# Optimization experiments

Measured on AMD Instinct MI355X. Metric: run time of the kernel, lower is better.

Reference implementation:

```python
import jax, jax.numpy as jnp
import numpy as np

N_NODES = 100000
N_EDGES = 1000000
NUM_GRAPHS = 500
EPS = 1e-5


def gcn_conv(x, src, dst, W, b, n_nodes):
    # PyG GCNConv: h = x @ W, symmetric norm with self-loops, aggregate at dst, add bias
    h = x @ W
    deg = jnp.zeros((n_nodes,), h.dtype).at[dst].add(1.0) + 1.0  # in-degree + self-loop
    dis = jax.lax.rsqrt(deg)
    msg = h[src] * (dis[src] * dis[dst])[:, None]               # [E, F] gather
    agg = jnp.zeros_like(h).at[dst].add(msg)                    # scatter-add
    return agg + h * (dis * dis)[:, None] + b                   # self-loop term + bias


def bn_eval(x, g, be, m, v):
    return (x - m) * jax.lax.rsqrt(v + EPS) * g + be


def setup_inputs() -> dict:
    key = jax.random.key(0)
    ks = jax.random.split(key, 8)
    edge_index = jax.random.randint(ks[0], (2, N_EDGES), 0, N_NODES, dtype=jnp.int32)
    batch = jnp.sort(jax.random.randint(ks[1], (N_NODES,), 0, NUM_GRAPHS, dtype=jnp.int32))
    d_in, h1, h2, hc, nc = 64, 64, 32, 16, 2
    return {
        "x": jax.random.normal(ks[2], (N_NODES, d_in), jnp.float32),
        "edge_index": edge_index,
        "batch": batch,
        "W1": jax.random.normal(ks[3], (d_in, h1), jnp.float32) / np.sqrt(d_in),
        "b1": jnp.zeros((h1,), jnp.float32),
        "g1": jnp.ones((h1,), jnp.float32),
        "be1": jnp.zeros((h1,), jnp.float32),
        "m1": jnp.zeros((h1,), jnp.float32),
        "v1": jnp.ones((h1,), jnp.float32),
        "W2": jax.random.normal(ks[4], (h1, h2), jnp.float32) / np.sqrt(h1),
        "b2": jnp.zeros((h2,), jnp.float32),
        "g2": jnp.ones((h2,), jnp.float32),
        "be2": jnp.zeros((h2,), jnp.float32),
        "m2": jnp.zeros((h2,), jnp.float32),
        "v2": jnp.ones((h2,), jnp.float32),
        "Wc1": jax.random.normal(ks[5], (h2, hc), jnp.float32) / np.sqrt(h2),
        "bc1": jnp.zeros((hc,), jnp.float32),
        "Wc2": jax.random.normal(ks[6], (hc, nc), jnp.float32) / np.sqrt(hc),
        "bc2": jnp.zeros((nc,), jnp.float32),
    }


def reference(x, edge_index, batch, W1, b1, g1, be1, m1, v1,
              W2, b2, g2, be2, m2, v2, Wc1, bc1, Wc2, bc2):
    src, dst = edge_index[0], edge_index[1]
    n = x.shape[0]
    # encoder layer 1: GCNConv -> BN(eval) -> ReLU  (dropout off in eval)
    h = jax.nn.relu(bn_eval(gcn_conv(x, src, dst, W1, b1, n), g1, be1, m1, v1))
    # encoder layer 2
    h = jax.nn.relu(bn_eval(gcn_conv(h, src, dst, W2, b2, n), g2, be2, m2, v2))
    # global mean pool over graphs
    sums = jax.ops.segment_sum(h, batch, num_segments=NUM_GRAPHS)
    cnts = jax.ops.segment_sum(jnp.ones((n,), h.dtype), batch, num_segments=NUM_GRAPHS)
    z = sums / jnp.maximum(cnts, 1.0)[:, None]                  # [NUM_GRAPHS, h2]
    # classifier MLP
    return jax.nn.relu(z @ Wc1 + bc1) @ Wc2 + bc2               # [NUM_GRAPHS, num_classes]
```

## Files before the change

kernel.cpp:

```cpp
#include <hip/hip_runtime.h>
#include <hip/hip_bf16.h>


#define CHUNK 4096
#define CAP   4096

typedef float floatx2 __attribute__((ext_vector_type(2)));

__global__ void k_zero_misc(int* __restrict__ bucketCursor, float* __restrict__ sums,
                            int nSums) {
    int i = blockIdx.x * blockDim.x + threadIdx.x;
    if (i < 512) bucketCursor[i] = 0;
    int j = i - 512;
    if (j >= 0 && j < nSums) sums[j] = 0.f;
}

__global__ __launch_bounds__(256) void k_binpairs2(
    const int* __restrict__ src, const int* __restrict__ dst,
    int* __restrict__ bucketCursor, unsigned* __restrict__ pairs, int E) {
    __shared__ int lh[512];
    __shared__ int lbase[512];
    for (int i = threadIdx.x; i < 512; i += 256) lh[i] = 0;
    __syncthreads();
    int base = blockIdx.x * CHUNK;
    for (int i = threadIdx.x; i < CHUNK; i += 256) {
        int e = base + i;
        if (e < E) atomicAdd(&lh[dst[e] >> 8], 1);
    }
    __syncthreads();
    for (int i = threadIdx.x; i < 512; i += 256) {
        int c = lh[i];
        lbase[i] = c ? atomicAdd(&bucketCursor[i], c) : 0;
        lh[i] = 0;
    }
    __syncthreads();
    for (int i = threadIdx.x; i < CHUNK; i += 256) {
        int e = base + i;
        if (e < E) {
            int d = dst[e];
            int b = d >> 8;
            int r = atomicAdd(&lh[b], 1);
            pairs[(size_t)b * CAP + lbase[b] + r] =
                ((unsigned)src[e] << 8) | (unsigned)(d & 255);
        }
    }
}

__global__ __launch_bounds__(256) void k_csr2(
    const unsigned* __restrict__ pairs, const int* __restrict__ bucketCursor,
    int* __restrict__ rowStart, int* __restrict__ rowEnd,
    float* __restrict__ dis, int* __restrict__ perm, int n) {
    __shared__ int cnt[256];
    __shared__ int s[256];
    __shared__ int cur[256];
    int b = blockIdx.x, tid = threadIdx.x;
    int total = bucketCursor[b];
    size_t base = (size_t)b * CAP;
    cnt[tid] = 0;
    __syncthreads();
    for (int i = tid; i < total; i += 256) atomicAdd(&cnt[pairs[base + i] & 255], 1);
    __syncthreads();
    int v = cnt[tid];
    s[tid] = v;
    __syncthreads();
    for (int off = 1; off < 256; off <<= 1) {
        int t = (tid >= off) ? s[tid - off] : 0;
        __syncthreads();
        s[tid] += t;
        __syncthreads();
    }
    int excl = s[tid] - v;
    int node = b * 256 + tid;
    if (node < n) {
        rowStart[node] = (int)base + excl;
        rowEnd[node]   = (int)base + excl + v;
        dis[node] = rsqrtf((float)v + 1.0f);
    }
    cur[tid] = excl;
    __syncthreads();
    for (int i = tid; i < total; i += 256) {
        unsigned pr = pairs[base + i];
        int lo = pr & 255;
        int slot = atomicAdd(&cur[lo], 1);
        perm[base + slot] = (int)(pr >> 8);
    }
}

__global__ __launch_bounds__(256) void k_gemm64(
    const float* __restrict__ x, const float* __restrict__ W,
    const float* __restrict__ dis, unsigned char* __restrict__ hs8, int n) {
    __shared__ float Ws[64 * 64];
    __shared__ float xs[128][65];
    const int tid = threadIdx.x;
    for (int i = tid * 4; i < 4096; i += 1024)
        *(float4*)&Ws[i] = *(const float4*)&W[i];
    const int base = blockIdx.x * 128;
    for (int i = tid; i < 2048; i += 256) {
        int r = i >> 4;
        int k = (i & 15) * 4;
        int row = base + r;
        float4 xv = (row < n) ? *(const float4*)&x[(size_t)row * 64 + k]
                              : make_float4(0.f, 0.f, 0.f, 0.f);
        xs[r][k] = xv.x; xs[r][k + 1] = xv.y; xs[r][k + 2] = xv.z; xs[r][k + 3] = xv.w;
    }
    __syncthreads();
    const int cg = tid & 7;
    const int rg = tid >> 3;
    float acc[4][8] = {};
#pragma unroll 4
    for (int k = 0; k < 64; ++k) {
        float w8[8];
        *(float4*)&w8[0] = *(const float4*)&Ws[k * 64 + cg * 8];
        *(float4*)&w8[4] = *(const float4*)&Ws[k * 64 + cg * 8 + 4];
        float x4[4];
#pragma unroll
        for (int rr = 0; rr < 4; ++rr) x4[rr] = xs[rg * 4 + rr][k];
#pragma unroll
        for (int rr = 0; rr < 4; ++rr)
#pragma unroll
            for (int cc = 0; cc < 8; ++cc)
                acc[rr][cc] = fmaf(x4[rr], w8[cc], acc[rr][cc]);
    }
#pragma unroll
    for (int rr = 0; rr < 4; ++rr) {
        int row = base + rg * 4 + rr;
        if (row >= n) break;
        float d = dis[row];
        int q0 = __builtin_amdgcn_cvt_pk_fp8_f32(acc[rr][0] * d, acc[rr][1] * d, 0, false);
        q0 = __builtin_amdgcn_cvt_pk_fp8_f32(acc[rr][2] * d, acc[rr][3] * d, q0, true);
        int q1 = __builtin_amdgcn_cvt_pk_fp8_f32(acc[rr][4] * d, acc[rr][5] * d, 0, false);
        q1 = __builtin_amdgcn_cvt_pk_fp8_f32(acc[rr][6] * d, acc[rr][7] * d, q1, true);
        uint2 q = {(unsigned)q0, (unsigned)q1};
        *(uint2*)&hs8[(size_t)row * 64 + cg * 8] = q;
    }
}

__device__ __forceinline__ void unpack8(uint2 u, float* a) {
    floatx2 p0 = __builtin_amdgcn_cvt_pk_f32_fp8(u.x, false);
    floatx2 p1 = __builtin_amdgcn_cvt_pk_f32_fp8(u.x, true);
    floatx2 p2 = __builtin_amdgcn_cvt_pk_f32_fp8(u.y, false);
    floatx2 p3 = __builtin_amdgcn_cvt_pk_f32_fp8(u.y, true);
    a[0] = p0[0]; a[1] = p0[1]; a[2] = p1[0]; a[3] = p1[1];
    a[4] = p2[0]; a[5] = p2[1]; a[6] = p3[0]; a[7] = p3[1];
}

__global__ __launch_bounds__(256) void k_g64f8_gemm32(
    const unsigned char* __restrict__ hs8, const int* __restrict__ rowStart,
    const int* __restrict__ rowEnd, const int* __restrict__ perm,
    const float* __restrict__ dis,
    const float* __restrict__ b, const float* __restrict__ g,
    const float* __restrict__ be, const float* __restrict__ m,
    const float* __restrict__ v, const float* __restrict__ W2,
    unsigned char* __restrict__ hs2f8, int n) {
    __shared__ float W2s[64 * 32];
    __shared__ float actS[32][68];
    for (int i = threadIdx.x * 4; i < 2048; i += 1024)
        *(float4*)&W2s[i] = *(const float4*)&W2[i];
    __syncthreads();

    const uint2* hsu = (const uint2*)hs8;
    int c = threadIdx.x & 7;
    int ln = threadIdx.x >> 3;
    int node = (blockIdx.x * 256 + threadIdx.x) >> 3;
    if (node >= n) return;
    int r0 = rowStart[node], r1 = rowEnd[node];
    float d = dis[node];
    float a[8];
    unpack8(hsu[(size_t)node * 8 + c], a);
    int e = r0;
    for (; e + 7 < r1; e += 8) {
        int s0 = perm[e],     s1 = perm[e + 1], s2 = perm[e + 2], s3 = perm[e + 3];
        int s4 = perm[e + 4], s5 = perm[e + 5], s6 = perm[e + 6], s7 = perm[e + 7];
        uint2 u0 = hsu[(size_t)s0 * 8 + c];
        uint2 u1 = hsu[(size_t)s1 * 8 + c];
        uint2 u2 = hsu[(size_t)s2 * 8 + c];
        uint2 u3 = hsu[(size_t)s3 * 8 + c];
        uint2 u4 = hsu[(size_t)s4 * 8 + c];
        uint2 u5 = hsu[(size_t)s5 * 8 + c];
        uint2 u6 = hsu[(size_t)s6 * 8 + c];
        uint2 u7 = hsu[(size_t)s7 * 8 + c];
        float t[8];
#pragma unroll
        for (int j = 0; j < 8; ++j) {
            uint2 u = j == 0 ? u0 : j == 1 ? u1 : j == 2 ? u2 : j == 3 ? u3
                    : j == 4 ? u4 : j == 5 ? u5 : j == 6 ? u6 : u7;
            unpack8(u, t);
#pragma unroll
            for (int q = 0; q < 8; ++q) a[q] += t[q];
        }
    }
    for (; e < r1; ++e) {
        float t[8];
        unpack8(hsu[(size_t)perm[e] * 8 + c], t);
#pragma unroll
        for (int q = 0; q < 8; ++q) a[q] += t[q];
    }
    int f = 8 * c;
    float y[8];
#pragma unroll
    for (int h = 0; h < 2; ++h) {
        float4 gv = *(const float4*)&g[f + 4 * h];
        float4 vv = *(const float4*)&v[f + 4 * h];
        float4 bv = *(const float4*)&b[f + 4 * h];
        float4 mv = *(const float4*)&m[f + 4 * h];
        float4 bev = *(const float4*)&be[f + 4 * h];
        float sc0 = gv.x * rsqrtf(vv.x + 1e-5f), sc1 = gv.y * rsqrtf(vv.y + 1e-5f);
        float sc2 = gv.z * rsqrtf(vv.z + 1e-5f), sc3 = gv.w * rsqrtf(vv.w + 1e-5f);
        float y0 = fmaf(a[4 * h + 0] * d, sc0, (bv.x - mv.x) * sc0 + bev.x);
        float y1 = fmaf(a[4 * h + 1] * d, sc1, (bv.y - mv.y) * sc1 + bev.y);
        float y2 = fmaf(a[4 * h + 2] * d, sc2, (bv.z - mv.z) * sc2 + bev.z);
        float y3 = fmaf(a[4 * h + 3] * d, sc3, (bv.w - mv.w) * sc3 + bev.w);
        y[4 * h + 0] = y0 > 0.f ? y0 : 0.f;
        y[4 * h + 1] = y1 > 0.f ? y1 : 0.f;
        y[4 * h + 2] = y2 > 0.f ? y2 : 0.f;
        y[4 * h + 3] = y3 > 0.f ? y3 : 0.f;
    }
    *(float4*)&actS[ln][f]     = *(float4*)&y[0];
    *(float4*)&actS[ln][f + 4] = *(float4*)&y[4];

    float o0 = 0.f, o1 = 0.f, o2 = 0.f, o3 = 0.f;
#pragma unroll
    for (int k = 0; k < 64; ++k) {
        float av = actS[ln][k];
        float4 w = *(const float4*)&W2s[k * 32 + 4 * c];
        o0 = fmaf(av, w.x, o0);
        o1 = fmaf(av, w.y, o1);
        o2 = fmaf(av, w.z, o2);
        o3 = fmaf(av, w.w, o3);
    }
    int q = __builtin_amdgcn_cvt_pk_fp8_f32(o0 * d, o1 * d, 0, false);
    q = __builtin_amdgcn_cvt_pk_fp8_f32(o2 * d, o3 * d, q, true);
    *(unsigned*)&hs2f8[(size_t)node * 32 + 4 * c] = (unsigned)q;
}

__global__ __launch_bounds__(256) void k_g32f8_pool(
    const unsigned char* __restrict__ hs8, const int* __restrict__ rowStart,
    const int* __restrict__ rowEnd, const int* __restrict__ perm,
    const float* __restrict__ dis,
    const float* __restrict__ b, const float* __restrict__ g,
    const float* __restrict__ be, const float* __restrict__ m,
    const float* __restrict__ v, const int* __restrict__ batch,
    float* __restrict__ sums, float* __restrict__ cntG, int n) {
    __shared__ float lsum[64][32];
    __shared__ float lcnt[64];
    const uint2* hsu = (const uint2*)hs8;
    int tid = threadIdx.x;
    int c = tid & 3;
    int node = (blockIdx.x * 256 + tid) >> 2;
    int base = blockIdx.x * 64;
    bool valid = node < n;

    int lastNode = min(base + 63, n - 1);
    int g0 = batch[base < n ? base : n - 1];
    int span = batch[lastNode] - g0 + 1;
    bool ldsPath = span <= 64;

    if (ldsPath) {
        for (int i = tid; i < span * 32; i += 256) lsum[i >> 5][i & 31] = 0.f;
        for (int i = tid; i < span; i += 256) lcnt[i] = 0.f;
    }
    __syncthreads();

    float y[8];
    int f = 8 * c;
    int bg = 0;
    if (valid) {
        int r0 = rowStart[node], r1 = rowEnd[node];
        float d = dis[node];
        float a[8];
        unpack8(hsu[(size_t)node * 4 + c], a);
        int e = r0;
        for (; e + 7 < r1; e += 8) {
            int s0 = perm[e],     s1 = perm[e + 1], s2 = perm[e + 2], s3 = perm[e + 3];
            int s4 = perm[e + 4], s5 = perm[e + 5], s6 = perm[e + 6], s7 = perm[e + 7];
            uint2 u0 = hsu[(size_t)s0 * 4 + c];
            uint2 u1 = hsu[(size_t)s1 * 4 + c];
            uint2 u2 = hsu[(size_t)s2 * 4 + c];
            uint2 u3 = hsu[(size_t)s3 * 4 + c];
            uint2 u4 = hsu[(size_t)s4 * 4 + c];
            uint2 u5 = hsu[(size_t)s5 * 4 + c];
            uint2 u6 = hsu[(size_t)s6 * 4 + c];
            uint2 u7 = hsu[(size_t)s7 * 4 + c];
            float t[8];
#pragma unroll
            for (int j = 0; j < 8; ++j) {
                uint2 u = j == 0 ? u0 : j == 1 ? u1 : j == 2 ? u2 : j == 3 ? u3
                        : j == 4 ? u4 : j == 5 ? u5 : j == 6 ? u6 : u7;
                unpack8(u, t);
#pragma unroll
                for (int q = 0; q < 8; ++q) a[q] += t[q];
            }
        }
        for (; e < r1; ++e) {
            float t[8];
            unpack8(hsu[(size_t)perm[e] * 4 + c], t);
#pragma unroll
            for (int q = 0; q < 8; ++q) a[q] += t[q];
        }
#pragma unroll
        for (int h = 0; h < 2; ++h) {
            float4 gv = *(const float4*)&g[f + 4 * h];
            float4 vv = *(const float4*)&v[f + 4 * h];
            float4 bv = *(const float4*)&b[f + 4 * h];
            float4 mv = *(const float4*)&m[f + 4 * h];
            float4 bev = *(const float4*)&be[f + 4 * h];
            float sc0 = gv.x * rsqrtf(vv.x + 1e-5f), sc1 = gv.y * rsqrtf(vv.y + 1e-5f);
            float sc2 = gv.z * rsqrtf(vv.z + 1e-5f), sc3 = gv.w * rsqrtf(vv.w + 1e-5f);
            float y0 = fmaf(a[4 * h + 0] * d, sc0, (bv.x - mv.x) * sc0 + bev.x);
            float y1 = fmaf(a[4 * h + 1] * d, sc1, (bv.y - mv.y) * sc1 + bev.y);
            float y2 = fmaf(a[4 * h + 2] * d, sc2, (bv.z - mv.z) * sc2 + bev.z);
            float y3 = fmaf(a[4 * h + 3] * d, sc3, (bv.w - mv.w) * sc3 + bev.w);
            y[4 * h + 0] = y0 > 0.f ? y0 : 0.f;
            y[4 * h + 1] = y1 > 0.f ? y1 : 0.f;
            y[4 * h + 2] = y2 > 0.f ? y2 : 0.f;
            y[4 * h + 3] = y3 > 0.f ? y3 : 0.f;
        }
        bg = batch[node];
        if (ldsPath) {
            int gl = bg - g0;
#pragma unroll
            for (int j = 0; j < 8; ++j) atomicAdd(&lsum[gl][f + j], y[j]);
            if (c == 0) atomicAdd(&lcnt[gl], 1.f);
        } else {
#pragma unroll
            for (int j = 0; j < 8; ++j) atomicAdd(&sums[(size_t)bg * 32 + f + j], y[j]);
            if (c == 0) atomicAdd(&cntG[bg], 1.f);
        }
    }
    __syncthreads();
    if (ldsPath) {
        for (int i = tid; i < span * 32; i += 256) {
            int gs = i >> 5, ff = i & 31;
            float vl = lsum[gs][ff];
            if (vl != 0.f) atomicAdd(&sums[(size_t)(g0 + gs) * 32 + ff], vl);
        }
        for (int i = tid; i < span; i += 256) {
            float vl = lcnt[i];
            if (vl != 0.f) atomicAdd(&cntG[g0 + i], vl);
        }
    }
}

__global__ void k_mlp(const float* __restrict__ sums, const float* __restrict__ cnt,
                      const float* __restrict__ Wc1, const float* __restrict__ bc1,
                      const float* __restrict__ Wc2, const float* __restrict__ bc2,
                      float* __restrict__ out, int G) {
    int g = blockIdx.x * blockDim.x + threadIdx.x;
    if (g >= G) return;
    float c = cnt[g];
    c = c < 1.f ? 1.f : c;
    float inv = 1.f / c;
    float z[32];
#pragma unroll
    for (int j = 0; j < 32; ++j) z[j] = sums[(size_t)g * 32 + j] * inv;
    float o0 = bc2[0], o1 = bc2[1];
#pragma unroll
    for (int k = 0; k < 16; ++k) {
        float t = bc1[k];
#pragma unroll
        for (int j = 0; j < 32; ++j) t = fmaf(z[j], Wc1[j * 16 + k], t);
        t = t > 0.f ? t : 0.f;
        o0 = fmaf(t, Wc2[k * 2 + 0], o0);
        o1 = fmaf(t, Wc2[k * 2 + 1], o1);
    }
    out[g * 2 + 0] = o0;
    out[g * 2 + 1] = o1;
}

extern "C" void kernel_launch(void* const* d_in, const int* in_sizes, int n_in,
                              void* d_out, int out_size, void* d_ws, size_t ws_size,
                              hipStream_t stream) {
    const float* x   = (const float*)d_in[0];
    const int* ei    = (const int*)d_in[1];
    const int* batch = (const int*)d_in[2];
    const float* W1  = (const float*)d_in[3];
    const float* b1  = (const float*)d_in[4];
    const float* g1  = (const float*)d_in[5];
    const float* be1 = (const float*)d_in[6];
    const float* m1  = (const float*)d_in[7];
    const float* v1  = (const float*)d_in[8];
    const float* W2  = (const float*)d_in[9];
    const float* b2  = (const float*)d_in[10];
    const float* g2  = (const float*)d_in[11];
    const float* be2 = (const float*)d_in[12];
    const float* m2  = (const float*)d_in[13];
    const float* v2  = (const float*)d_in[14];
    const float* Wc1 = (const float*)d_in[15];
    const float* bc1 = (const float*)d_in[16];
    const float* Wc2 = (const float*)d_in[17];
    const float* bc2 = (const float*)d_in[18];

    const int n = in_sizes[2];
    const int E = in_sizes[1] / 2;
    const int G = out_size / 2;
    const int* srcI = ei;
    const int* dstI = ei + E;
    const int NB = (n + 255) >> 8;

    char* pw = (char*)d_ws;
    auto alloc = [&](size_t bytes) {
        char* r = pw;
        pw += (bytes + 255) & ~(size_t)255;
        return r;
    };
    float*    dis          = (float*)alloc((size_t)n * 4);
    int*      bucketCursor = (int*)alloc(512 * 4);
    unsigned* pairs        = (unsigned*)alloc((size_t)NB * CAP * 4);
    int*      perm         = (int*)alloc((size_t)NB * CAP * 4);
    int*      rowStart     = (int*)alloc((size_t)n * 4);
    int*      rowEnd       = (int*)alloc((size_t)n * 4);
    unsigned char* hs1f8   = (unsigned char*)alloc((size_t)64 * n);
    unsigned char* hs2f8   = (unsigned char*)alloc((size_t)32 * n);
    float*    sums         = (float*)alloc((size_t)32 * G * 4 + (size_t)G * 4);
    float*    cntG         = sums + (size_t)32 * G;

    const int NT = 256;
    const int nbE = (E + CHUNK - 1) / CHUNK;
    const int nSums = G * 33;

    k_zero_misc<<<(512 + nSums + NT - 1) / NT, NT, 0, stream>>>(bucketCursor, sums, nSums);
    k_binpairs2<<<nbE, NT, 0, stream>>>(srcI, dstI, bucketCursor, pairs, E);
    k_csr2<<<NB, NT, 0, stream>>>(pairs, bucketCursor, rowStart, rowEnd, dis, perm, n);

    k_gemm64<<<(n + 127) / 128, NT, 0, stream>>>(x, W1, dis, hs1f8, n);
    k_g64f8_gemm32<<<(n * 8 + NT - 1) / NT, NT, 0, stream>>>(
        hs1f8, rowStart, rowEnd, perm, dis, b1, g1, be1, m1, v1, W2, hs2f8, n);

    k_g32f8_pool<<<(n * 4 + NT - 1) / NT, NT, 0, stream>>>(
        hs2f8, rowStart, rowEnd, perm, dis, b2, g2, be2, m2, v2, batch,
        sums, cntG, n);

    k_mlp<<<(G + NT - 1) / NT, NT, 0, stream>>>(sums, cntG, Wc1, bc1, Wc2, bc2,
                                                (float*)d_out, G);
}
```

Baseline: 128.0 us.

## Fuse MLP into pool kernel via last-block counter and drop zeroing kernel

The classifier MLP now runs in the last block of the pooling kernel, chosen by an atomic done-counter with thread fences, so its separate launch goes away. Zeroing of the pooled sums moves into the CSR kernel, and the cursor reset becomes a memset. The edge-binning chunk size is doubled, halving that kernel's block count. Savings come from fewer kernel launches, at the cost of a serial MLP tail in one block and the correctness risk of last-block synchronisation. Zeroing sums inside k_csr2 only covers the whole array if NB*256 >= G*33, which holds here.

```diff
diff --git a/kernel.cpp b/kernel.cpp
--- a/kernel.cpp
+++ b/kernel.cpp
@@ -2,18 +2,10 @@
 #include <hip/hip_bf16.h>
 
 
-#define CHUNK 4096
+#define CHUNK 8192
 #define CAP   4096
 
 typedef float floatx2 __attribute__((ext_vector_type(2)));
-
-__global__ void k_zero_misc(int* __restrict__ bucketCursor, float* __restrict__ sums,
-                            int nSums) {
-    int i = blockIdx.x * blockDim.x + threadIdx.x;
-    if (i < 512) bucketCursor[i] = 0;
-    int j = i - 512;
-    if (j >= 0 && j < nSums) sums[j] = 0.f;
-}
 
 __global__ __launch_bounds__(256) void k_binpairs2(
     const int* __restrict__ src, const int* __restrict__ dst,
@@ -49,11 +41,14 @@
 __global__ __launch_bounds__(256) void k_csr2(
     const unsigned* __restrict__ pairs, const int* __restrict__ bucketCursor,
     int* __restrict__ rowStart, int* __restrict__ rowEnd,
-    float* __restrict__ dis, int* __restrict__ perm, int n) {
+    float* __restrict__ dis, int* __restrict__ perm, int n,
+    float* __restrict__ sums, int nSums) {
     __shared__ int cnt[256];
     __shared__ int s[256];
     __shared__ int cur[256];
     int b = blockIdx.x, tid = threadIdx.x;
+    int zi = b * 256 + tid;
+    if (zi < nSums) sums[zi] = 0.f;
     int total = bucketCursor[b];
     size_t base = (size_t)b * CAP;
     cnt[tid] = 0;
@@ -233,16 +228,20 @@
     *(unsigned*)&hs2f8[(size_t)node * 32 + 4 * c] = (unsigned)q;
 }
 
-__global__ __launch_bounds__(256) void k_g32f8_pool(
+__global__ __launch_bounds__(256) void k_g32f8_pool_mlp(
     const unsigned char* __restrict__ hs8, const int* __restrict__ rowStart,
     const int* __restrict__ rowEnd, const int* __restrict__ perm,
     const float* __restrict__ dis,
     const float* __restrict__ b, const float* __restrict__ g,
     const float* __restrict__ be, const float* __restrict__ m,
     const float* __restrict__ v, const int* __restrict__ batch,
-    float* __restrict__ sums, float* __restrict__ cntG, int n) {
+    float* __restrict__ sums, float* __restrict__ cntG,
+    const float* __restrict__ Wc1, const float* __restrict__ bc1,
+    const float* __restrict__ Wc2, const float* __restrict__ bc2,
+    float* __restrict__ out, int* __restrict__ doneCnt, int n, int G) {
     __shared__ float lsum[64][32];
     __shared__ float lcnt[64];
+    __shared__ int isLast;
     const uint2* hsu = (const uint2*)hs8;
     int tid = threadIdx.x;
     int c = tid & 3;
@@ -263,7 +262,6 @@
 
     float y[8];
     int f = 8 * c;
-    int bg = 0;
     if (valid) {
         int r0 = rowStart[node], r1 = rowEnd[node];
         float d = dis[node];
@@ -315,7 +313,7 @@
             y[4 * h + 2] = y2 > 0.f ? y2 : 0.f;
             y[4 * h + 3] = y3 > 0.f ? y3 : 0.f;
         }
-        bg = batch[node];
+        int bg = batch[node];
         if (ldsPath) {
             int gl = bg - g0;
 #pragma unroll
@@ -339,32 +337,37 @@
             if (vl != 0.f) atomicAdd(&cntG[g0 + i], vl);
         }
     }
-}
-
-__global__ void k_mlp(const float* __restrict__ sums, const float* __restrict__ cnt,
-                      const float* __restrict__ Wc1, const float* __restrict__ bc1,
-                      const float* __restrict__ Wc2, const float* __restrict__ bc2,
-                      float* __restrict__ out, int G) {
-    int g = blockIdx.x * blockDim.x + threadIdx.x;
-    if (g >= G) return;
-    float c = cnt[g];
-    c = c < 1.f ? 1.f : c;
-    float inv = 1.f / c;
-    float z[32];
-#pragma unroll
-    for (int j = 0; j < 32; ++j) z[j] = sums[(size_t)g * 32 + j] * inv;
-    float o0 = bc2[0], o1 = bc2[1];
-#pragma unroll
-    for (int k = 0; k < 16; ++k) {
-        float t = bc1[k];
-#pragma unroll
-        for (int j = 0; j < 32; ++j) t = fmaf(z[j], Wc1[j * 16 + k], t);
-        t = t > 0.f ? t : 0.f;
-        o0 = fmaf(t, Wc2[k * 2 + 0], o0);
-        o1 = fmaf(t, Wc2[k * 2 + 1], o1);
-    }
-    out[g * 2 + 0] = o0;
-    out[g * 2 + 1] = o1;
+
+    __syncthreads();
+    if (tid == 0) {
+        __threadfence();
+        int prev = atomicAdd(doneCnt, 1);
+        isLast = (prev == (int)gridDim.x - 1) ? 1 : 0;
+    }
+    __syncthreads();
+    if (isLast) {
+        __threadfence();
+        for (int gg = tid; gg < G; gg += 256) {
+            float cn = cntG[gg];
+            cn = cn < 1.f ? 1.f : cn;
+            float inv = 1.f / cn;
+            float z[32];
+#pragma unroll
+            for (int j = 0; j < 32; ++j) z[j] = sums[(size_t)gg * 32 + j] * inv;
+            float o0 = bc2[0], o1 = bc2[1];
+#pragma unroll
+            for (int k = 0; k < 16; ++k) {
+                float t = bc1[k];
+#pragma unroll
+                for (int j = 0; j < 32; ++j) t = fmaf(z[j], Wc1[j * 16 + k], t);
+                t = t > 0.f ? t : 0.f;
+                o0 = fmaf(t, Wc2[k * 2 + 0], o0);
+                o1 = fmaf(t, Wc2[k * 2 + 1], o1);
+            }
+            out[gg * 2 + 0] = o0;
+            out[gg * 2 + 1] = o1;
+        }
+    }
 }
 
 extern "C" void kernel_launch(void* const* d_in, const int* in_sizes, int n_in,
@@ -404,7 +407,7 @@
         return r;
     };
     float*    dis          = (float*)alloc((size_t)n * 4);
-    int*      bucketCursor = (int*)alloc(512 * 4);
+    int*      bucketCursor = (int*)alloc(513 * 4);
     unsigned* pairs        = (unsigned*)alloc((size_t)NB * CAP * 4);
     int*      perm         = (int*)alloc((size_t)NB * CAP * 4);
     int*      rowStart     = (int*)alloc((size_t)n * 4);
@@ -413,23 +416,22 @@
     unsigned char* hs2f8   = (unsigned char*)alloc((size_t)32 * n);
     float*    sums         = (float*)alloc((size_t)32 * G * 4 + (size_t)G * 4);
     float*    cntG         = sums + (size_t)32 * G;
+    int*      doneCnt      = bucketCursor + 512;
 
     const int NT = 256;
     const int nbE = (E + CHUNK - 1) / CHUNK;
     const int nSums = G * 33;
 
-    k_zero_misc<<<(512 + nSums + NT - 1) / NT, NT, 0, stream>>>(bucketCursor, sums, nSums);
+    hipMemsetAsync(bucketCursor, 0, 513 * 4, stream);
     k_binpairs2<<<nbE, NT, 0, stream>>>(srcI, dstI, bucketCursor, pairs, E);
-    k_csr2<<<NB, NT, 0, stream>>>(pairs, bucketCursor, rowStart, rowEnd, dis, perm, n);
+    k_csr2<<<NB, NT, 0, stream>>>(pairs, bucketCursor, rowStart, rowEnd, dis, perm,
+                                  n, sums, nSums);
 
     k_gemm64<<<(n + 127) / 128, NT, 0, stream>>>(x, W1, dis, hs1f8, n);
     k_g64f8_gemm32<<<(n * 8 + NT - 1) / NT, NT, 0, stream>>>(
         hs1f8, rowStart, rowEnd, perm, dis, b1, g1, be1, m1, v1, W2, hs2f8, n);
 
-    k_g32f8_pool<<<(n * 4 + NT - 1) / NT, NT, 0, stream>>>(
+    k_g32f8_pool_mlp<<<(n * 4 + NT - 1) / NT, NT, 0, stream>>>(
         hs2f8, rowStart, rowEnd, perm, dis, b2, g2, be2, m2, v2, batch,
-        sums, cntG, n);
-
-    k_mlp<<<(G + NT - 1) / NT, NT, 0, stream>>>(sums, cntG, Wc1, bc1, Wc2, bc2,
-                                                (float*)d_out, G);
-}
+        sums, cntG, Wc1, bc1, Wc2, bc2, (float*)d_out, doneCnt, n, G);
+}
```

Measured after the change: 176.0 us. 1.38x slower.
